# Kernel optimization log

Measured on AMD Instinct MI355X. Metric: run time of the kernel, lower is better.

## Reference

```python
import jax, jax.numpy as jnp
import numpy as np
from jax import lax

NMS_THRESH = 0.5
BN_EPS = 1e-5
TO_REMOVE = 1.0  # neural-motifs box convention (+1 in width/height)


def nms_overlaps(boxes):
    # boxes: [N, C, 4] xyxy -> per-class pairwise IoU [N, N, C]
    x1 = jnp.maximum(boxes[:, None, :, 0], boxes[None, :, :, 0])
    y1 = jnp.maximum(boxes[:, None, :, 1], boxes[None, :, :, 1])
    x2 = jnp.minimum(boxes[:, None, :, 2], boxes[None, :, :, 2])
    y2 = jnp.minimum(boxes[:, None, :, 3], boxes[None, :, :, 3])
    inter = jnp.clip(x2 - x1 + TO_REMOVE, 0.0) * jnp.clip(y2 - y1 + TO_REMOVE, 0.0)
    area = (boxes[:, :, 2] - boxes[:, :, 0] + TO_REMOVE) * (boxes[:, :, 3] - boxes[:, :, 1] + TO_REMOVE)  # [N,C]
    union = area[:, None, :] + area[None, :, :] - inter
    return inter / union


def greedy_nms_labels(obj_dists, is_overlap):
    # faithful port of nms_per_cls: iterative argmax + per-class suppression
    N, C = obj_dists.shape
    scores = jax.nn.softmax(obj_dists, axis=-1)
    scores = scores.at[:, 0].set(-1.0)  # kill background column

    def step(carry, _):
        scores, labels = carry
        flat = jnp.argmax(scores)          # row-major, same as np.unravel_index
        box_ind = flat // C
        cls_ind = flat % C
        labels = labels.at[box_ind].set(cls_ind.astype(jnp.int32))
        ov = is_overlap[box_ind, :, cls_ind]  # [N] bool
        col = jnp.where(ov, 0.0, scores[:, cls_ind])
        scores = scores.at[:, cls_ind].set(col)
        scores = scores.at[box_ind, :].set(-1.0)
        return (scores, labels), None

    (_, labels), _ = lax.scan(step, (scores, jnp.zeros(N, jnp.int32)), None, length=N)
    return labels


def setup_inputs() -> dict:
    key = jax.random.key(0)
    ks = jax.random.split(key, 16)
    N, C, D, E, H, P = 400, 151, 4096, 200, 512, 128
    x = jax.random.normal(ks[0], (N, D), jnp.float32)
    predict_logits = jax.random.normal(ks[1], (N, C), jnp.float32) * 2.0
    pos_input = jax.random.uniform(ks[2], (N, 9), jnp.float32)
    xy = jax.random.uniform(ks[3], (N, C, 2), jnp.float32) * 800.0
    wh = jax.random.uniform(ks[4], (N, C, 2), jnp.float32) * 200.0 + 1.0
    boxes_per_cls = jnp.concatenate([xy, xy + wh], axis=-1)
    sc = lambda k, sh: jax.random.normal(k, sh, jnp.float32) * np.float32(1.0 / np.sqrt(sh[0]))
    return {
        'x': x,
        'predict_logits': predict_logits,
        'pos_input': pos_input,
        'boxes_per_cls': boxes_per_cls,
        'obj_embed_w': jax.random.normal(ks[5], (C, E), jnp.float32) * 0.1,
        'obj_embed2_w': jax.random.normal(ks[6], (C, E), jnp.float32) * 0.1,
        'w_pos1': sc(ks[7], (9, 32)), 'b_pos1': jnp.zeros(32, jnp.float32),
        'bn_gamma': jnp.ones(32, jnp.float32), 'bn_beta': jnp.zeros(32, jnp.float32),
        'bn_mean': jnp.zeros(32, jnp.float32), 'bn_var': jnp.ones(32, jnp.float32),
        'w_pos2': sc(ks[8], (32, P)), 'b_pos2': jnp.zeros(P, jnp.float32),
        'w_lin': sc(ks[9], (D + E + P, H)), 'b_lin': jnp.zeros(H, jnp.float32),
        'w_out': sc(ks[10], (H, C)), 'b_out': jnp.zeros(C, jnp.float32),
        'w_fc': sc(ks[11], (D + E + P, H)), 'b_fc': jnp.zeros(H, jnp.float32),
    }


def reference(x, predict_logits, pos_input, boxes_per_cls, obj_embed_w, obj_embed2_w,
              w_pos1, b_pos1, bn_gamma, bn_beta, bn_mean, bn_var, w_pos2, b_pos2,
              w_lin, b_lin, w_out, b_out, w_fc, b_fc):
    # sgdet inference path of VTransEFeaturePE.forward
    obj_embed = jax.nn.softmax(predict_logits, axis=-1) @ obj_embed_w           # [N,E]
    h = pos_input @ w_pos1 + b_pos1                                             # Linear(9,32)
    h = (h - bn_mean) / jnp.sqrt(bn_var + BN_EPS) * bn_gamma + bn_beta          # BN eval
    pos_embed = jax.nn.relu(h @ w_pos2 + b_pos2)                                # [N,128]
    rep = jnp.concatenate([x, obj_embed, pos_embed], axis=-1)                   # [N,4424]
    obj_dists = (rep @ w_lin + b_lin) @ w_out + b_out                           # [N,C]
    is_overlap = nms_overlaps(boxes_per_cls) >= NMS_THRESH                      # [N,N,C]
    obj_preds = greedy_nms_labels(obj_dists, is_overlap)                        # [N] int32
    obj_embed2 = obj_embed2_w[obj_preds]                                        # [N,E]
    obj_rel_rep = jnp.concatenate([x, pos_embed, obj_embed2], axis=-1)
    edge_ctx = jax.nn.relu(obj_rel_rep @ w_fc + b_fc)                           # [N,H]
    return (obj_dists, obj_preds, edge_ctx)
```

## Files before the change

kernel.cpp:

```cpp
#include <hip/hip_runtime.h>
#include <hip/hip_bf16.h>
#include <stdint.h>

#define NB 400
#define NC 151
#define DX 4096
#define DE 200
#define DP 128
#define DH 512
#define KREP 4424
#define TAILW 328
#define MPAD 416
#define SPLITK 8
#define TILES1 139
#define TILES2 132
#define SLOTS 7
#define SKSTRIDE 152

__device__ __forceinline__ uint32_t f2ord(float f) {
  uint32_t u = __float_as_uint(f);
  return (u & 0x80000000u) ? ~u : (u | 0x80000000u);
}

__global__ __launch_bounds__(256) void k_embed(
    const float* __restrict__ logits, const float* __restrict__ obj_embed_w,
    const float* __restrict__ pos_input, const float* __restrict__ w_pos1,
    const float* __restrict__ b_pos1, const float* __restrict__ bn_gamma,
    const float* __restrict__ bn_beta, const float* __restrict__ bn_mean,
    const float* __restrict__ bn_var, const float* __restrict__ w_pos2,
    const float* __restrict__ b_pos2, float* __restrict__ tail1) {
  int r = blockIdx.x, t = threadIdx.x;
  if (r >= NB) {
    if (t < TAILW) tail1[r * TAILW + t] = 0.f;
    return;
  }
  __shared__ float p[NC];
  __shared__ float red[256];
  __shared__ float hb[32];

  float v = (t < NC) ? logits[r * NC + t] : -INFINITY;
  red[t] = v; __syncthreads();
  for (int s = 128; s > 0; s >>= 1) { if (t < s) red[t] = fmaxf(red[t], red[t + s]); __syncthreads(); }
  float m = red[0]; __syncthreads();
  float e = (t < NC) ? expf(v - m) : 0.f;
  red[t] = e; __syncthreads();
  for (int s = 128; s > 0; s >>= 1) { if (t < s) red[t] += red[t + s]; __syncthreads(); }
  float sum = red[0];
  if (t < NC) p[t] = e / sum;

  if (t < 32) {
    float acc = b_pos1[t];
    for (int k = 0; k < 9; k++) acc += pos_input[r * 9 + k] * w_pos1[k * 32 + t];
    acc = (acc - bn_mean[t]) / sqrtf(bn_var[t] + 1e-5f) * bn_gamma[t] + bn_beta[t];
    hb[t] = acc;
  }
  __syncthreads();

  if (t < DE) {
    float acc = 0.f;
    for (int k = 0; k < NC; k++) acc += p[k] * obj_embed_w[k * DE + t];
    tail1[r * TAILW + t] = acc;
  }
  if (t < DP) {
    float acc = b_pos2[t];
    for (int k = 0; k < 32; k++) acc += hb[k] * w_pos2[k * DP + t];
    tail1[r * TAILW + DE + t] = fmaxf(acc, 0.f);
  }
}

__device__ __forceinline__ void gemm_body(
    const float* __restrict__ x, const float* __restrict__ tail,
    const float* __restrict__ w, float* __restrict__ part,
    int bid, int tiles, int toff) {
  __shared__ __align__(16) float As[32][36];
  __shared__ __align__(16) float Bs[32][68];
  int tid = threadIdx.x;
  int n0 = (bid & 7) * 64, m0 = ((bid >> 3) % 13) * 32;
  int z = bid / 104;
  int tbeg = (z * tiles) / SPLITK, tend = ((z + 1) * tiles) / SPLITK;
  int ty = tid >> 4, tx = tid & 15;
  int a_r = tid >> 3, a_c = (tid & 7) << 2;
  int b_r = tid >> 4, b_c = (tid & 15) << 2;
  float4 acc0 = {0, 0, 0, 0}, acc1 = {0, 0, 0, 0};

  auto loadA = [&](int t) -> float4 {
    int k = t * 32 + a_c;
    int row = m0 + a_r;
    float4 v = {0, 0, 0, 0};
    if (k < KREP) {
      if (k < DX) { if (row < NB) v = *(const float4*)&x[(size_t)row * DX + k]; }
      else v = *(const float4*)&tail[row * TAILW + toff + (k - DX)];
    }
    return v;
  };
  auto loadB = [&](int t, int roff) -> float4 {
    int k = t * 32 + b_r + roff;
    float4 v = {0, 0, 0, 0};
    if (k < KREP) v = *(const float4*)&w[(size_t)k * DH + n0 + b_c];
    return v;
  };

  float4 pa = loadA(tbeg), pb0 = loadB(tbeg, 0), pb1 = loadB(tbeg, 16);
  for (int t = tbeg; t < tend; t++) {
    __syncthreads();
    *(float4*)&As[a_r][a_c] = pa;
    *(float4*)&Bs[b_r][b_c] = pb0;
    *(float4*)&Bs[b_r + 16][b_c] = pb1;
    __syncthreads();
    if (t + 1 < tend) { pa = loadA(t + 1); pb0 = loadB(t + 1, 0); pb1 = loadB(t + 1, 16); }
#pragma unroll
    for (int k4 = 0; k4 < 8; k4++) {
      float4 a0 = *(float4*)&As[ty * 2][k4 * 4];
      float4 a1 = *(float4*)&As[ty * 2 + 1][k4 * 4];
#pragma unroll
      for (int j = 0; j < 4; j++) {
        float4 bv = *(float4*)&Bs[k4 * 4 + j][tx * 4];
        float av0 = (&a0.x)[j], av1 = (&a1.x)[j];
        acc0.x += av0 * bv.x; acc0.y += av0 * bv.y; acc0.z += av0 * bv.z; acc0.w += av0 * bv.w;
        acc1.x += av1 * bv.x; acc1.y += av1 * bv.y; acc1.z += av1 * bv.z; acc1.w += av1 * bv.w;
      }
    }
  }
  int row0 = m0 + ty * 2, col = n0 + tx * 4;
  float* base = part + (size_t)z * NB * DH;
  if (row0 < NB)     *(float4*)&base[row0 * DH + col] = acc0;
  if (row0 + 1 < NB) *(float4*)&base[(row0 + 1) * DH + col] = acc1;
}

__global__ __launch_bounds__(256) void k_g1ov(
    const float* __restrict__ x, const float* __restrict__ tail1,
    const float* __restrict__ w_lin, float* __restrict__ part,
    const float* __restrict__ boxes, uint64_t* __restrict__ ov_bits) {
  int bid = blockIdx.x;
  if (bid >= 832) {
    int c = bid - 832;
    int t = threadIdx.x;
    __shared__ float4 bx[NB];
    const float4* bp4 = (const float4*)boxes;
    for (int j = t; j < NB; j += 256) bx[j] = bp4[j * NC + c];
    __syncthreads();
    int wave = t >> 6, lane = t & 63;
    for (int b = wave; b < NB; b += 4) {
      float4 A = bx[b];
      float areaA = (A.z - A.x + 1.f) * (A.w - A.y + 1.f);
      for (int chunk = 0; chunk < 7; chunk++) {
        int j = chunk * 64 + lane;
        bool ov = false;
        if (j < NB) {
          float4 B = bx[j];
          float x1 = fmaxf(A.x, B.x), y1 = fmaxf(A.y, B.y);
          float x2 = fminf(A.z, B.z), y2 = fminf(A.w, B.w);
          float iw = fmaxf(x2 - x1 + 1.f, 0.f), ih = fmaxf(y2 - y1 + 1.f, 0.f);
          float inter = iw * ih;
          float areaB = (B.z - B.x + 1.f) * (B.w - B.y + 1.f);
          ov = (inter / (areaA + areaB - inter)) >= 0.5f;
        }
        uint64_t mask = __ballot(ov);
        if (lane == 0) ov_bits[((size_t)(b * NC + c) << 3) + chunk] = mask;
      }
    }
    return;
  }
  gemm_body(x, tail1, w_lin, part, bid, TILES1, 0);
}

__global__ __launch_bounds__(256) void k_dists(
    const float* __restrict__ part, const float* __restrict__ b_lin,
    const float* __restrict__ w_out, const float* __restrict__ b_out,
    float* __restrict__ out_dists, uint64_t* __restrict__ skeys) {
  int r = blockIdx.x, t = threadIdx.x;
  __shared__ float h[DH];
  __shared__ float red[256];
  __shared__ float sval[NC];
  float s0 = b_lin[t], s1 = b_lin[t + 256];
#pragma unroll
  for (int z = 0; z < SPLITK; z++) {
    const float* pr = part + ((size_t)z * NB + r) * DH;
    s0 += pr[t]; s1 += pr[t + 256];
  }
  h[t] = s0; h[t + 256] = s1;
  __syncthreads();

  float acc = -INFINITY;
  if (t < NC) {
    acc = b_out[t];
    for (int k = 0; k < DH; k++) acc += h[k] * w_out[k * NC + t];
    out_dists[r * NC + t] = acc;
  }
  red[t] = (t < NC) ? acc : -INFINITY; __syncthreads();
  for (int s = 128; s > 0; s >>= 1) { if (t < s) red[t] = fmaxf(red[t], red[t + s]); __syncthreads(); }
  float mx = red[0]; __syncthreads();
  float e = (t < NC) ? expf(acc - mx) : 0.f;
  red[t] = e; __syncthreads();
  for (int s = 128; s > 0; s >>= 1) { if (t < s) red[t] += red[t + s]; __syncthreads(); }
  float sum = red[0];
  if (t < NC) sval[t] = e / sum;
  __syncthreads();

  if (t >= 1 && t < NC) {
    float v = sval[t];
    int rank = 0;
    for (int c2 = 1; c2 < NC; c2++) {
      float v2 = sval[c2];
      rank += (v2 > v) || (v2 == v && c2 < t);
    }
    skeys[(size_t)r * SKSTRIDE + rank] =
        ((uint64_t)f2ord(v) << 17) | ((uint64_t)(511 - r) << 8) | (uint64_t)t;
  }
}

__global__ __launch_bounds__(256) void k_nms_g2a(
    const uint64_t* __restrict__ ov_bits, const uint64_t* __restrict__ skeys,
    int* __restrict__ labels_g, float* __restrict__ out_preds,
    const float* __restrict__ x, const float* __restrict__ tail1,
    const float* __restrict__ w_fc, float* __restrict__ part) {
  if (blockIdx.x > 0) {
    gemm_body(x, tail1, w_fc, part, blockIdx.x - 1, TILES2, DE);
    return;
  }
  if (threadIdx.x >= 64) return;
  int lane = threadIdx.x;
  uint64_t cand[SLOTS];
  uint64_t supp0[SLOTS], supp1[SLOTS], supp2[SLOTS];
  int depth[SLOTS];
  bool removed[SLOTS];
  int reszmin[SLOTS];

#pragma unroll
  for (int s = 0; s < SLOTS; s++) {
    int r = s * 64 + lane;
    supp0[s] = supp1[s] = supp2[s] = 0;
    depth[s] = 0; removed[s] = false; reszmin[s] = 255;
    if (r < NB) {
      cand[s] = skeys[(size_t)r * SKSTRIDE];
      labels_g[r] = 0; out_preds[r] = 0.f;
    } else cand[s] = 0;
  }

  auto apply = [&](int b, int c, const uint64_t* ow) {
#pragma unroll
    for (int s = 0; s < SLOTS; s++) {
      int r = s * 64 + lane;
      if (r == b) {
        removed[s] = true; reszmin[s] = 255;
        cand[s] = ((uint64_t)0x407FFFFFu << 17) | ((uint64_t)(511 - r) << 8);
        labels_g[b] = c; out_preds[b] = (float)c;
      } else if ((ow[s] >> lane) & 1) {
        if (removed[s]) {
          if (c < reszmin[s]) reszmin[s] = c;
          cand[s] = ((uint64_t)0x80000000u << 17) | ((uint64_t)(511 - r) << 8)
                    | (uint64_t)reszmin[s];
        } else {
          uint64_t bit = 1ull << (c & 63);
          if (c < 64) supp0[s] |= bit; else if (c < 128) supp1[s] |= bit; else supp2[s] |= bit;
          if ((int)(cand[s] & 0xFF) == c) {
            int d = depth[s] + 1;
            uint64_t k = 0;
            for (; d < 150; d++) {
              k = skeys[(size_t)r * SKSTRIDE + d];
              int col = (int)(k & 0xFF);
              uint64_t mm = (col < 64) ? supp0[s] : ((col < 128) ? supp1[s] : supp2[s]);
              if (!((mm >> (col & 63)) & 1)) break;
            }
            if (d >= 150)
              k = ((uint64_t)0x80000000u << 17) | ((uint64_t)(511 - r) << 8) | 1ull;
            depth[s] = d; cand[s] = k;
          }
        }
      }
    }
  };

  auto cswap = [](uint64_t& a, uint64_t& b) {
    uint64_t hi = a > b ? a : b, lo = a > b ? b : a; a = hi; b = lo;
  };

  int picked = 0;
  while (picked < NB) {
    uint64_t k0 = 0, k1 = 0, k2 = 0, k3 = 0;
#pragma unroll
    for (int s = 0; s < SLOTS; s++) {
      uint64_t v = cand[s];
      if (v > k0)      { k3 = k2; k2 = k1; k1 = k0; k0 = v; }
      else if (v > k1) { k3 = k2; k2 = k1; k1 = v; }
      else if (v > k2) { k3 = k2; k2 = v; }
      else if (v > k3) { k3 = v; }
    }
#pragma unroll
    for (int off = 1; off < 64; off <<= 1) {
      uint64_t p0 = (uint64_t)__shfl_xor((unsigned long long)k0, off, 64);
      uint64_t p1 = (uint64_t)__shfl_xor((unsigned long long)k1, off, 64);
      uint64_t p2 = (uint64_t)__shfl_xor((unsigned long long)k2, off, 64);
      uint64_t p3 = (uint64_t)__shfl_xor((unsigned long long)k3, off, 64);
      uint64_t t0 = k0 > p3 ? k0 : p3;
      uint64_t t1 = k1 > p2 ? k1 : p2;
      uint64_t t2 = k2 > p1 ? k2 : p1;
      uint64_t t3 = k3 > p0 ? k3 : p0;
      cswap(t0, t2); cswap(t1, t3); cswap(t0, t1); cswap(t2, t3);
      k0 = t0; k1 = t1; k2 = t2; k3 = t3;
    }
    int b0 = 511 - (int)((k0 >> 8) & 0x1FF), c0 = (int)(k0 & 0xFF);
    int b1 = 511 - (int)((k1 >> 8) & 0x1FF), c1 = (int)(k1 & 0xFF);
    int b2 = 511 - (int)((k2 >> 8) & 0x1FF), c2 = (int)(k2 & 0xFF);
    int b3 = 511 - (int)((k3 >> 8) & 0x1FF), c3 = (int)(k3 & 0xFF);
    int npick = NB - picked; if (npick > 4) npick = 4;

    int pi = lane >> 3, pw = lane & 7;
    uint64_t wv = 0;
    if (pi < npick && pw < 7) {
      int bb = (pi == 0) ? b0 : (pi == 1) ? b1 : (pi == 2) ? b2 : b3;
      int cc = (pi == 0) ? c0 : (pi == 1) ? c1 : (pi == 2) ? c2 : c3;
      wv = ov_bits[(((size_t)(bb * NC + cc)) << 3) + pw];
    }
    auto ovb = [&](int ii, int bj) -> bool {
      bool f = ((lane >> 3) == ii) && ((lane & 7) == (bj >> 6)) && ((wv >> (bj & 63)) & 1);
      return __ballot(f) != 0ull;
    };
    uint32_t v1 = (uint32_t)(k1 >> 17), v2 = (uint32_t)(k2 >> 17), v3 = (uint32_t)(k3 >> 17);
    int napply = 1;
    if (npick >= 2 && v1 > 0x80000000u && !(c1 == c0 && ovb(0, b1))) {
      napply = 2;
      if (npick >= 3 && v2 > 0x80000000u &&
          !(c2 == c0 && ovb(0, b2)) && !(c2 == c1 && ovb(1, b2))) {
        napply = 3;
        if (npick >= 4 && v3 > 0x80000000u &&
            !(c3 == c0 && ovb(0, b3)) && !(c3 == c1 && ovb(1, b3)) &&
            !(c3 == c2 && ovb(2, b3)))
          napply = 4;
      }
    }

    uint64_t ow[SLOTS];
#pragma unroll
    for (int s = 0; s < SLOTS; s++) ow[s] = (uint64_t)__shfl((unsigned long long)wv, s, 64);
    apply(b0, c0, ow);
    if (napply >= 2) {
#pragma unroll
      for (int s = 0; s < SLOTS; s++) ow[s] = (uint64_t)__shfl((unsigned long long)wv, 8 + s, 64);
      apply(b1, c1, ow);
    }
    if (napply >= 3) {
#pragma unroll
      for (int s = 0; s < SLOTS; s++) ow[s] = (uint64_t)__shfl((unsigned long long)wv, 16 + s, 64);
      apply(b2, c2, ow);
    }
    if (napply >= 4) {
#pragma unroll
      for (int s = 0; s < SLOTS; s++) ow[s] = (uint64_t)__shfl((unsigned long long)wv, 24 + s, 64);
      apply(b3, c3, ow);
    }
    picked += napply;
  }
}

__global__ __launch_bounds__(256) void k_final(
    const float* __restrict__ emb2, const int* __restrict__ labels,
    const float* __restrict__ w_fc, const float* __restrict__ part,
    const float* __restrict__ b_fc, float* __restrict__ out_edge) {
  __shared__ __align__(16) float As[32][36];
  __shared__ __align__(16) float Bs[32][68];
  int tid = threadIdx.x;
  int n0 = blockIdx.x * 64, m0 = blockIdx.y * 32;
  int ty = tid >> 4, tx = tid & 15;
  int a_r = tid >> 3, a_c = (tid & 7) << 2;
  int b_r = tid >> 4, b_c = (tid & 15) << 2;
  float4 acc0 = {0, 0, 0, 0}, acc1 = {0, 0, 0, 0};
  int row_a = m0 + a_r;
  int lab = (row_a < NB) ? labels[row_a] : 0;

  auto loadA = [&](int t) -> float4 {
    int kk = t * 32 + a_c;
    float4 v = {0, 0, 0, 0};
    if (kk < DE && row_a < NB) v = *(const float4*)&emb2[(size_t)lab * DE + kk];
    return v;
  };
  auto loadB = [&](int t, int roff) -> float4 {
    int kk = t * 32 + b_r + roff;
    float4 v = {0, 0, 0, 0};
    if (kk < DE) v = *(const float4*)&w_fc[(size_t)(DX + DP + kk) * DH + n0 + b_c];
    return v;
  };

  float4 pa = loadA(0), pb0 = loadB(0, 0), pb1 = loadB(0, 16);
  for (int t = 0; t < 7; t++) {
    __syncthreads();
    *(float4*)&As[a_r][a_c] = pa;
    *(float4*)&Bs[b_r][b_c] = pb0;
    *(float4*)&Bs[b_r + 16][b_c] = pb1;
    __syncthreads();
    if (t + 1 < 7) { pa = loadA(t + 1); pb0 = loadB(t + 1, 0); pb1 = loadB(t + 1, 16); }
#pragma unroll
    for (int k4 = 0; k4 < 8; k4++) {
      float4 a0 = *(float4*)&As[ty * 2][k4 * 4];
      float4 a1 = *(float4*)&As[ty * 2 + 1][k4 * 4];
#pragma unroll
      for (int j = 0; j < 4; j++) {
        float4 bv = *(float4*)&Bs[k4 * 4 + j][tx * 4];
        float av0 = (&a0.x)[j], av1 = (&a1.x)[j];
        acc0.x += av0 * bv.x; acc0.y += av0 * bv.y; acc0.z += av0 * bv.z; acc0.w += av0 * bv.w;
        acc1.x += av1 * bv.x; acc1.y += av1 * bv.y; acc1.z += av1 * bv.z; acc1.w += av1 * bv.w;
      }
    }
  }
  int row0 = m0 + ty * 2, col = n0 + tx * 4;
#pragma unroll
  for (int z = 0; z < SPLITK; z++) {
    if (row0 < NB) {
      float4 p = *(const float4*)&part[((size_t)z * NB + row0) * DH + col];
      acc0.x += p.x; acc0.y += p.y; acc0.z += p.z; acc0.w += p.w;
    }
    if (row0 + 1 < NB) {
      float4 p = *(const float4*)&part[((size_t)z * NB + row0 + 1) * DH + col];
      acc1.x += p.x; acc1.y += p.y; acc1.z += p.z; acc1.w += p.w;
    }
  }
  float4 bv = *(const float4*)&b_fc[col];
  if (row0 < NB) {
    float4 r;
    r.x = fmaxf(acc0.x + bv.x, 0.f); r.y = fmaxf(acc0.y + bv.y, 0.f);
    r.z = fmaxf(acc0.z + bv.z, 0.f); r.w = fmaxf(acc0.w + bv.w, 0.f);
    *(float4*)&out_edge[row0 * DH + col] = r;
  }
  if (row0 + 1 < NB) {
    float4 r;
    r.x = fmaxf(acc1.x + bv.x, 0.f); r.y = fmaxf(acc1.y + bv.y, 0.f);
    r.z = fmaxf(acc1.z + bv.z, 0.f); r.w = fmaxf(acc1.w + bv.w, 0.f);
    *(float4*)&out_edge[(row0 + 1) * DH + col] = r;
  }
}

extern "C" void kernel_launch(void* const* d_in, const int* in_sizes, int n_in,
                              void* d_out, int out_size, void* d_ws, size_t ws_size,
                              hipStream_t stream) {
  const float* x            = (const float*)d_in[0];
  const float* logits       = (const float*)d_in[1];
  const float* pos_input    = (const float*)d_in[2];
  const float* boxes        = (const float*)d_in[3];
  const float* obj_embed_w  = (const float*)d_in[4];
  const float* obj_embed2_w = (const float*)d_in[5];
  const float* w_pos1       = (const float*)d_in[6];
  const float* b_pos1       = (const float*)d_in[7];
  const float* bn_gamma     = (const float*)d_in[8];
  const float* bn_beta      = (const float*)d_in[9];
  const float* bn_mean      = (const float*)d_in[10];
  const float* bn_var       = (const float*)d_in[11];
  const float* w_pos2       = (const float*)d_in[12];
  const float* b_pos2       = (const float*)d_in[13];
  const float* w_lin        = (const float*)d_in[14];
  const float* b_lin        = (const float*)d_in[15];
  const float* w_out        = (const float*)d_in[16];
  const float* b_out        = (const float*)d_in[17];
  const float* w_fc         = (const float*)d_in[18];
  const float* b_fc         = (const float*)d_in[19];

  float* ws         = (float*)d_ws;
  float* tail1      = ws;
  int* labels       = (int*)(tail1 + MPAD * TAILW);
  uint64_t* skeys   = (uint64_t*)(labels + MPAD);
  uint64_t* ov_bits = skeys + (size_t)NB * SKSTRIDE;
  float* part       = (float*)(ov_bits + (size_t)NB * NC * 8);

  float* out       = (float*)d_out;
  float* out_dists = out;
  float* out_preds = out + NB * NC;
  float* out_edge  = out + NB * NC + NB;

  k_embed<<<MPAD, 256, 0, stream>>>(logits, obj_embed_w, pos_input, w_pos1, b_pos1,
                                    bn_gamma, bn_beta, bn_mean, bn_var, w_pos2, b_pos2,
                                    tail1);
  k_g1ov<<<983, 256, 0, stream>>>(x, tail1, w_lin, part, boxes, ov_bits);
  k_dists<<<NB, 256, 0, stream>>>(part, b_lin, w_out, b_out, out_dists, skeys);
  k_nms_g2a<<<833, 256, 0, stream>>>(ov_bits, skeys, labels, out_preds,
                                     x, tail1, w_fc, part);
  k_final<<<dim3(8, 13), 256, 0, stream>>>(obj_embed2_w, labels, w_fc, part,
                                           b_fc, out_edge);
}
```

Before: 627.5 us.

## Rewrite greedy NMS as single-pick loop with LDS-cached overlap rows

Replaces the batched multi-pick (top-4 per step) greedy NMS with a simple one-pick-per-step argmax loop. Each box's overlap bitmask row for its current best class and its suppression masks now live in shared memory, so the serial chain mostly avoids global loads. Shared memory is pooled across the GEMM and NMS roles so the NMS block can take a larger allocation. The trade is 400 serial steps instead of fewer batched ones, each with a full wave reduction and a cached or global row fetch.

After: 778.4 us. 1.24x slower.

```diff
diff --git a/kernel.cpp b/kernel.cpp
--- a/kernel.cpp
+++ b/kernel.cpp
@@ -14,7 +14,7 @@
 #define SPLITK 8
 #define TILES1 139
 #define TILES2 132
-#define SLOTS 7
+#define NGB 832
 #define SKSTRIDE 152
 
 __device__ __forceinline__ uint32_t f2ord(float f) {
@@ -71,9 +71,7 @@
 __device__ __forceinline__ void gemm_body(
     const float* __restrict__ x, const float* __restrict__ tail,
     const float* __restrict__ w, float* __restrict__ part,
-    int bid, int tiles, int toff) {
-  __shared__ __align__(16) float As[32][36];
-  __shared__ __align__(16) float Bs[32][68];
+    int bid, int tiles, int toff, float* As, float* Bs) {
   int tid = threadIdx.x;
   int n0 = (bid & 7) * 64, m0 = ((bid >> 3) % 13) * 32;
   int z = bid / 104;
@@ -103,18 +101,18 @@
   float4 pa = loadA(tbeg), pb0 = loadB(tbeg, 0), pb1 = loadB(tbeg, 16);
   for (int t = tbeg; t < tend; t++) {
     __syncthreads();
-    *(float4*)&As[a_r][a_c] = pa;
-    *(float4*)&Bs[b_r][b_c] = pb0;
-    *(float4*)&Bs[b_r + 16][b_c] = pb1;
+    *(float4*)&As[a_r * 36 + a_c] = pa;
+    *(float4*)&Bs[b_r * 68 + b_c] = pb0;
+    *(float4*)&Bs[(b_r + 16) * 68 + b_c] = pb1;
     __syncthreads();
     if (t + 1 < tend) { pa = loadA(t + 1); pb0 = loadB(t + 1, 0); pb1 = loadB(t + 1, 16); }
 #pragma unroll
     for (int k4 = 0; k4 < 8; k4++) {
-      float4 a0 = *(float4*)&As[ty * 2][k4 * 4];
-      float4 a1 = *(float4*)&As[ty * 2 + 1][k4 * 4];
+      float4 a0 = *(float4*)&As[(ty * 2) * 36 + k4 * 4];
+      float4 a1 = *(float4*)&As[(ty * 2 + 1) * 36 + k4 * 4];
 #pragma unroll
       for (int j = 0; j < 4; j++) {
-        float4 bv = *(float4*)&Bs[k4 * 4 + j][tx * 4];
+        float4 bv = *(float4*)&Bs[(k4 * 4 + j) * 68 + tx * 4];
         float av0 = (&a0.x)[j], av1 = (&a1.x)[j];
         acc0.x += av0 * bv.x; acc0.y += av0 * bv.y; acc0.z += av0 * bv.z; acc0.w += av0 * bv.w;
         acc1.x += av1 * bv.x; acc1.y += av1 * bv.y; acc1.z += av1 * bv.z; acc1.w += av1 * bv.w;
@@ -131,11 +129,12 @@
     const float* __restrict__ x, const float* __restrict__ tail1,
     const float* __restrict__ w_lin, float* __restrict__ part,
     const float* __restrict__ boxes, uint64_t* __restrict__ ov_bits) {
+  __shared__ __align__(16) char pool[13312];
   int bid = blockIdx.x;
-  if (bid >= 832) {
-    int c = bid - 832;
+  if (bid >= NGB) {
+    int c = bid - NGB;
     int t = threadIdx.x;
-    __shared__ float4 bx[NB];
+    float4* bx = (float4*)pool;
     const float4* bp4 = (const float4*)boxes;
     for (int j = t; j < NB; j += 256) bx[j] = bp4[j * NC + c];
     __syncthreads();
@@ -161,7 +160,8 @@
     }
     return;
   }
-  gemm_body(x, tail1, w_lin, part, bid, TILES1, 0);
+  gemm_body(x, tail1, w_lin, part, bid, TILES1, 0,
+            (float*)pool, (float*)(pool + 4608));
 }
 
 __global__ __launch_bounds__(256) void k_dists(
@@ -214,142 +214,107 @@
     int* __restrict__ labels_g, float* __restrict__ out_preds,
     const float* __restrict__ x, const float* __restrict__ tail1,
     const float* __restrict__ w_fc, float* __restrict__ part) {
+  __shared__ __align__(16) char pool[34816];
   if (blockIdx.x > 0) {
-    gemm_body(x, tail1, w_fc, part, blockIdx.x - 1, TILES2, DE);
+    gemm_body(x, tail1, w_fc, part, blockIdx.x - 1, TILES2, DE,
+              (float*)pool, (float*)(pool + 4608));
     return;
   }
-  if (threadIdx.x >= 64) return;
-  int lane = threadIdx.x;
-  uint64_t cand[SLOTS];
-  uint64_t supp0[SLOTS], supp1[SLOTS], supp2[SLOTS];
-  int depth[SLOTS];
-  bool removed[SLOTS];
-  int reszmin[SLOTS];
-
-#pragma unroll
-  for (int s = 0; s < SLOTS; s++) {
+  uint64_t* ovc   = (uint64_t*)pool;
+  uint64_t* suppL = (uint64_t*)(pool + 22400);
+  int*      ccol  = (int*)(pool + 33152);
+
+  int tid = threadIdx.x;
+  for (int i = tid; i < 448 * 3; i += 256) suppL[i] = 0;
+  for (int r = tid; r < NB; r += 256) {
+    labels_g[r] = 0; out_preds[r] = 0.f;
+    int hc = (int)(skeys[(size_t)r * SKSTRIDE] & 0xFF);
+    ccol[r] = hc;
+    const uint64_t* src = ov_bits + (((size_t)(r * NC + hc)) << 3);
+#pragma unroll
+    for (int k = 0; k < 7; k++) ovc[r * 7 + k] = src[k];
+  }
+  __syncthreads();
+  if (tid >= 64) return;
+  int lane = tid;
+
+  const uint64_t SENT = ((uint64_t)0x407FFFFFu << 17);
+  const uint64_t RESV = ((uint64_t)0x80000000u << 17);
+
+  uint64_t cand[7];
+  int depth[7], rmin[7];
+  uint32_t remm = 0;
+#pragma unroll
+  for (int s = 0; s < 7; s++) {
     int r = s * 64 + lane;
-    supp0[s] = supp1[s] = supp2[s] = 0;
-    depth[s] = 0; removed[s] = false; reszmin[s] = 255;
-    if (r < NB) {
-      cand[s] = skeys[(size_t)r * SKSTRIDE];
-      labels_g[r] = 0; out_preds[r] = 0.f;
-    } else cand[s] = 0;
-  }
-
-  auto apply = [&](int b, int c, const uint64_t* ow) {
-#pragma unroll
-    for (int s = 0; s < SLOTS; s++) {
+    cand[s] = (r < NB) ? skeys[(size_t)r * SKSTRIDE] : 0;
+    depth[s] = 0; rmin[s] = 255;
+  }
+
+  for (int step = 0; step < NB; step++) {
+    uint64_t best = cand[0];
+#pragma unroll
+    for (int s = 1; s < 7; s++) if (cand[s] > best) best = cand[s];
+#pragma unroll
+    for (int off = 1; off < 64; off <<= 1) {
+      uint64_t o = (uint64_t)__shfl_xor((unsigned long long)best, off, 64);
+      if (o > best) best = o;
+    }
+    int b = 511 - (int)((best >> 8) & 0x1FF);
+    int c = (int)(best & 0xFF);
+
+    uint64_t ow[7];
+    if (ccol[b] == c) {
+#pragma unroll
+      for (int k = 0; k < 7; k++) ow[k] = ovc[b * 7 + k];
+    } else {
+      uint64_t wv = 0;
+      if (lane < 7) wv = ov_bits[(((size_t)(b * NC + c)) << 3) + lane];
+#pragma unroll
+      for (int k = 0; k < 7; k++) ow[k] = (uint64_t)__shfl((unsigned long long)wv, k, 64);
+    }
+
+#pragma unroll
+    for (int s = 0; s < 7; s++) {
       int r = s * 64 + lane;
+      if (r >= NB) continue;
       if (r == b) {
-        removed[s] = true; reszmin[s] = 255;
-        cand[s] = ((uint64_t)0x407FFFFFu << 17) | ((uint64_t)(511 - r) << 8);
+        remm |= (1u << s); rmin[s] = 255;
+        cand[s] = SENT | ((uint64_t)(511 - r) << 8);
         labels_g[b] = c; out_preds[b] = (float)c;
       } else if ((ow[s] >> lane) & 1) {
-        if (removed[s]) {
-          if (c < reszmin[s]) reszmin[s] = c;
-          cand[s] = ((uint64_t)0x80000000u << 17) | ((uint64_t)(511 - r) << 8)
-                    | (uint64_t)reszmin[s];
+        if ((remm >> s) & 1) {
+          if (c < rmin[s]) rmin[s] = c;
+          cand[s] = RESV | ((uint64_t)(511 - r) << 8) | (uint64_t)rmin[s];
         } else {
-          uint64_t bit = 1ull << (c & 63);
-          if (c < 64) supp0[s] |= bit; else if (c < 128) supp1[s] |= bit; else supp2[s] |= bit;
-          if ((int)(cand[s] & 0xFF) == c) {
+          suppL[r * 3 + (c >> 6)] |= (1ull << (c & 63));
+          if ((int)(cand[s] & 0xFF) == c &&
+              (uint32_t)(cand[s] >> 17) > 0x80000000u) {
             int d = depth[s] + 1;
-            uint64_t k = 0;
+            uint64_t nk = 0;
             for (; d < 150; d++) {
-              k = skeys[(size_t)r * SKSTRIDE + d];
-              int col = (int)(k & 0xFF);
-              uint64_t mm = (col < 64) ? supp0[s] : ((col < 128) ? supp1[s] : supp2[s]);
-              if (!((mm >> (col & 63)) & 1)) break;
+              nk = skeys[(size_t)r * SKSTRIDE + d];
+              int col = (int)(nk & 0xFF);
+              if (!((suppL[r * 3 + (col >> 6)] >> (col & 63)) & 1)) break;
             }
-            if (d >= 150)
-              k = ((uint64_t)0x80000000u << 17) | ((uint64_t)(511 - r) << 8) | 1ull;
-            depth[s] = d; cand[s] = k;
+            depth[s] = d;
+            if (d >= 150) {
+              cand[s] = RESV | ((uint64_t)(511 - r) << 8) | 1ull;
+            } else {
+              cand[s] = nk;
+              int ncol = (int)(nk & 0xFF);
+              const uint64_t* src = ov_bits + (((size_t)(r * NC + ncol)) << 3);
+              uint64_t t0 = src[0], t1 = src[1], t2 = src[2], t3 = src[3],
+                       t4 = src[4], t5 = src[5], t6 = src[6];
+              ovc[r * 7 + 0] = t0; ovc[r * 7 + 1] = t1; ovc[r * 7 + 2] = t2;
+              ovc[r * 7 + 3] = t3; ovc[r * 7 + 4] = t4; ovc[r * 7 + 5] = t5;
+              ovc[r * 7 + 6] = t6;
+              ccol[r] = ncol;
+            }
           }
         }
       }
     }
-  };
-
-  auto cswap = [](uint64_t& a, uint64_t& b) {
-    uint64_t hi = a > b ? a : b, lo = a > b ? b : a; a = hi; b = lo;
-  };
-
-  int picked = 0;
-  while (picked < NB) {
-    uint64_t k0 = 0, k1 = 0, k2 = 0, k3 = 0;
-#pragma unroll
-    for (int s = 0; s < SLOTS; s++) {
-      uint64_t v = cand[s];
-      if (v > k0)      { k3 = k2; k2 = k1; k1 = k0; k0 = v; }
-      else if (v > k1) { k3 = k2; k2 = k1; k1 = v; }
-      else if (v > k2) { k3 = k2; k2 = v; }
-      else if (v > k3) { k3 = v; }
-    }
-#pragma unroll
-    for (int off = 1; off < 64; off <<= 1) {
-      uint64_t p0 = (uint64_t)__shfl_xor((unsigned long long)k0, off, 64);
-      uint64_t p1 = (uint64_t)__shfl_xor((unsigned long long)k1, off, 64);
-      uint64_t p2 = (uint64_t)__shfl_xor((unsigned long long)k2, off, 64);
-      uint64_t p3 = (uint64_t)__shfl_xor((unsigned long long)k3, off, 64);
-      uint64_t t0 = k0 > p3 ? k0 : p3;
-      uint64_t t1 = k1 > p2 ? k1 : p2;
-      uint64_t t2 = k2 > p1 ? k2 : p1;
-      uint64_t t3 = k3 > p0 ? k3 : p0;
-      cswap(t0, t2); cswap(t1, t3); cswap(t0, t1); cswap(t2, t3);
-      k0 = t0; k1 = t1; k2 = t2; k3 = t3;
-    }
-    int b0 = 511 - (int)((k0 >> 8) & 0x1FF), c0 = (int)(k0 & 0xFF);
-    int b1 = 511 - (int)((k1 >> 8) & 0x1FF), c1 = (int)(k1 & 0xFF);
-    int b2 = 511 - (int)((k2 >> 8) & 0x1FF), c2 = (int)(k2 & 0xFF);
-    int b3 = 511 - (int)((k3 >> 8) & 0x1FF), c3 = (int)(k3 & 0xFF);
-    int npick = NB - picked; if (npick > 4) npick = 4;
-
-    int pi = lane >> 3, pw = lane & 7;
-    uint64_t wv = 0;
-    if (pi < npick && pw < 7) {
-      int bb = (pi == 0) ? b0 : (pi == 1) ? b1 : (pi == 2) ? b2 : b3;
-      int cc = (pi == 0) ? c0 : (pi == 1) ? c1 : (pi == 2) ? c2 : c3;
-      wv = ov_bits[(((size_t)(bb * NC + cc)) << 3) + pw];
-    }
-    auto ovb = [&](int ii, int bj) -> bool {
-      bool f = ((lane >> 3) == ii) && ((lane & 7) == (bj >> 6)) && ((wv >> (bj & 63)) & 1);
-      return __ballot(f) != 0ull;
-    };
-    uint32_t v1 = (uint32_t)(k1 >> 17), v2 = (uint32_t)(k2 >> 17), v3 = (uint32_t)(k3 >> 17);
-    int napply = 1;
-    if (npick >= 2 && v1 > 0x80000000u && !(c1 == c0 && ovb(0, b1))) {
-      napply = 2;
-      if (npick >= 3 && v2 > 0x80000000u &&
-          !(c2 == c0 && ovb(0, b2)) && !(c2 == c1 && ovb(1, b2))) {
-        napply = 3;
-        if (npick >= 4 && v3 > 0x80000000u &&
-            !(c3 == c0 && ovb(0, b3)) && !(c3 == c1 && ovb(1, b3)) &&
-            !(c3 == c2 && ovb(2, b3)))
-          napply = 4;
-      }
-    }
-
-    uint64_t ow[SLOTS];
-#pragma unroll
-    for (int s = 0; s < SLOTS; s++) ow[s] = (uint64_t)__shfl((unsigned long long)wv, s, 64);
-    apply(b0, c0, ow);
-    if (napply >= 2) {
-#pragma unroll
-      for (int s = 0; s < SLOTS; s++) ow[s] = (uint64_t)__shfl((unsigned long long)wv, 8 + s, 64);
-      apply(b1, c1, ow);
-    }
-    if (napply >= 3) {
-#pragma unroll
-      for (int s = 0; s < SLOTS; s++) ow[s] = (uint64_t)__shfl((unsigned long long)wv, 16 + s, 64);
-      apply(b2, c2, ow);
-    }
-    if (napply >= 4) {
-#pragma unroll
-      for (int s = 0; s < SLOTS; s++) ow[s] = (uint64_t)__shfl((unsigned long long)wv, 24 + s, 64);
-      apply(b3, c3, ow);
-    }
-    picked += napply;
   }
 }
 
@@ -456,7 +421,7 @@
   float* ws         = (float*)d_ws;
   float* tail1      = ws;
   int* labels       = (int*)(tail1 + MPAD * TAILW);
-  uint64_t* skeys   = (uint64_t*)(labels + MPAD);
+  uint64_t* skeys   = (uint64_t*)(labels + 512);
   uint64_t* ov_bits = skeys + (size_t)NB * SKSTRIDE;
   float* part       = (float*)(ov_bits + (size_t)NB * NC * 8);
 
@@ -468,10 +433,10 @@
   k_embed<<<MPAD, 256, 0, stream>>>(logits, obj_embed_w, pos_input, w_pos1, b_pos1,
                                     bn_gamma, bn_beta, bn_mean, bn_var, w_pos2, b_pos2,
                                     tail1);
-  k_g1ov<<<983, 256, 0, stream>>>(x, tail1, w_lin, part, boxes, ov_bits);
+  k_g1ov<<<NGB + NC, 256, 0, stream>>>(x, tail1, w_lin, part, boxes, ov_bits);
   k_dists<<<NB, 256, 0, stream>>>(part, b_lin, w_out, b_out, out_dists, skeys);
-  k_nms_g2a<<<833, 256, 0, stream>>>(ov_bits, skeys, labels, out_preds,
-                                     x, tail1, w_fc, part);
+  k_nms_g2a<<<NGB + 1, 256, 0, stream>>>(ov_bits, skeys, labels, out_preds,
+                                         x, tail1, w_fc, part);
   k_final<<<dim3(8, 13), 256, 0, stream>>>(obj_embed2_w, labels, w_fc, part,
                                            b_fc, out_edge);
 }
```
